# Kernel optimization log

Hardware: AMD Instinct MI355X
Metric: run time of the kernel (lower is better)

Reference implementation:

```python
import jax, jax.numpy as jnp
import numpy as np

B, L, P, A, D = 64, 512, 64, 16, 512  # batch, seq_len, n_positions, n_actions, n_lstm


def setup_inputs() -> dict:
    key = jax.random.key(0)
    ks = jax.random.split(key, 6)
    F = P + A
    observations = jax.random.normal(ks[0], (B, L, P), jnp.float32)
    actions = jax.random.normal(ks[1], (B, L, A), jnp.float32)
    # xavier_normal init as in the torch module
    W_ci = jax.random.normal(ks[2], (F, D), jnp.float32) * np.float32(np.sqrt(2.0 / (F + D)))
    b_ci = jnp.zeros((D,), jnp.float32)
    R_ig = jax.random.normal(ks[3], (D, D), jnp.float32) * np.float32(np.sqrt(2.0 / (D + D)))
    b_ig = jnp.zeros((D,), jnp.float32)
    W_out = jax.random.normal(ks[4], (D, 1), jnp.float32) * np.float32(np.sqrt(2.0 / (D + 1)))
    b_out = jnp.zeros((1,), jnp.float32)
    return dict(observations=observations, actions=actions, W_ci=W_ci, b_ci=b_ci,
                R_ig=R_ig, b_ig=b_ig, W_out=W_out, b_out=b_out)


def reference(observations, actions, W_ci, b_ci, R_ig, b_ig, W_out, b_out):
    # Custom LSTM: forget gate = 1, output gate = 1, a_out = identity =>
    #   h_t = c_t = c_{t-1} + tanh(x_t @ W_ci + b_ci) * sigmoid(h_{t-1} @ R_ig + b_ig)
    x = jnp.concatenate([observations, actions], axis=-1)          # [B, L, F]
    ci = jnp.tanh(jnp.einsum('blf,fd->bld', x, W_ci) + b_ci)       # precompute cell input [B, L, D]
    ci_seq = jnp.swapaxes(ci, 0, 1)                                # [L, B, D] for scan
    h0 = jnp.zeros((x.shape[0], R_ig.shape[0]), x.dtype)

    def step(h, ci_t):
        ig = jax.nn.sigmoid(h @ R_ig + b_ig)
        h_new = h + ci_t * ig
        return h_new, h_new

    _, hs = jax.lax.scan(step, h0, ci_seq)                         # hs: [L, B, D]
    hs = jnp.swapaxes(hs, 0, 1)                                    # [B, L, D]
    return hs @ W_out + b_out                                      # [B, L, 1]
```

## Files before the change

kernel.cpp:

```cpp
#include <hip/hip_runtime.h>


#define B_  64
#define L_  512
#define P_  64
#define A_  16
#define D_  512
#define F_  80
#define CI_R 8

#define CI_BYTES   ((size_t)B_ * L_ * D_ * 2)
#define RP_BYTES   ((size_t)D_ * D_ * 2)
#define HBUF_UINTS (2 * B_ * 2 * 256)
#define PBANK      ((size_t)B_ * 2 * 256)
#define SPIN_CAP   65536

typedef _Float16 half2_t __attribute__((ext_vector_type(2)));
typedef unsigned int uintx4 __attribute__((ext_vector_type(4)));

__device__ __forceinline__ float dot2(unsigned int r, unsigned int h, float acc) {
    return __builtin_amdgcn_fdot2(__builtin_bit_cast(half2_t, h),
                                  __builtin_bit_cast(half2_t, r), acc, false);
}
__device__ __forceinline__ float dot4u(uintx4 r, uintx4 h, float acc) {
    acc = dot2(r.x, h.x, acc);
    acc = dot2(r.y, h.y, acc);
    acc = dot2(r.z, h.z, acc);
    acc = dot2(r.w, h.w, acc);
    return acc;
}
template<int CTRL>
__device__ __forceinline__ float dpp_mov(float v) {
    return __builtin_bit_cast(float, __builtin_amdgcn_update_dpp(
        0, __builtin_bit_cast(int, v), CTRL, 0xF, 0xF, true));
}

__device__ __forceinline__ unsigned int pk_f16(float a, float b) {
    return __builtin_bit_cast(unsigned int, __builtin_amdgcn_cvt_pkrtz(a, b));
}
__device__ __forceinline__ unsigned int ld_sc01(const unsigned int* p) {
    unsigned int v;
    asm volatile("global_load_dword %0, %1, off sc0 sc1\n\t"
                 "s_waitcnt vmcnt(0)" : "=v"(v) : "v"(p) : "memory");
    return v;
}
__device__ __forceinline__ void st_sc01(unsigned int* p, unsigned int v) {
    asm volatile("global_store_dword %0, %1, off sc0 sc1" :: "v"(p), "v"(v) : "memory");
}
__device__ __forceinline__ int swz4(int i) {
    return ((i >> 3) << 3) | ((i + (i >> 3)) & 7);
}

__global__ __launch_bounds__(256) void prep_kernel(const float* __restrict__ R,
        unsigned int* __restrict__ Rp, unsigned int* __restrict__ hbuf,
        float* __restrict__ out) {
    int id = blockIdx.x * 256 + threadIdx.x;
    int dw = id & 3;
    int U = id >> 2;
    int tid_s = U & 511;
    int m  = (U >> 9) & 31;
    int qq = U >> 14;
    int w = tid_s >> 6, l = tid_s & 63, r = l >> 3, g = l & 7;
    int hh = m >> 4, j = (m >> 2) & 3, c = m & 3;
    int d  = qq * 256 + (w * 8 + r) * 4 + j;
    int k0 = hh * 256 + (g & 3) * 64 + (g >> 2) * 32 + c * 8 + 2 * dw;
    half2_t v;
    v.x = (_Float16)R[k0 * D_ + d];
    v.y = (_Float16)R[(k0 + 1) * D_ + d];
    Rp[id] = __builtin_bit_cast(unsigned int, v);
    if (id < HBUF_UINTS) hbuf[id] = 0u;
    if (id < B_ * L_) out[id] = 0.f;
}

__global__ __launch_bounds__(256) void ci_kernel(const float* __restrict__ obs,
                                                 const float* __restrict__ act,
                                                 const float* __restrict__ W,
                                                 const float* __restrict__ bci,
                                                 unsigned short* __restrict__ ci) {
    __shared__ float xs[CI_R][F_];
    int row0 = blockIdx.x * CI_R;
    int tid = threadIdx.x;
    for (int idx = tid; idx < CI_R * F_; idx += 256) {
        int r = idx / F_, f = idx % F_;
        float v = (f < P_) ? obs[(size_t)(row0 + r) * P_ + f]
                           : act[(size_t)(row0 + r) * A_ + (f - P_)];
        xs[r][f] = v;
    }
    __syncthreads();
    int d0 = tid, d1 = tid + 256;
    float a0[CI_R], a1[CI_R];
    #pragma unroll
    for (int r = 0; r < CI_R; ++r) { a0[r] = 0.f; a1[r] = 0.f; }
    for (int f = 0; f < F_; ++f) {
        float w0 = W[f * D_ + d0];
        float w1 = W[f * D_ + d1];
        #pragma unroll
        for (int r = 0; r < CI_R; ++r) {
            float xv = xs[r][f];
            a0[r] += xv * w0;
            a1[r] += xv * w1;
        }
    }
    float b0 = bci[d0], b1 = bci[d1];
    #pragma unroll
    for (int r = 0; r < CI_R; ++r) {
        float z0 = a0[r] + b0, z1 = a1[r] + b1;
        float e0 = __expf(-2.f * __builtin_fabsf(z0));
        float e1 = __expf(-2.f * __builtin_fabsf(z1));
        float m0 = (1.f - e0) * __builtin_amdgcn_rcpf(1.f + e0);
        float m1 = (1.f - e1) * __builtin_amdgcn_rcpf(1.f + e1);
        float t0 = z0 < 0.f ? -m0 : m0;
        float t1 = z1 < 0.f ? -m1 : m1;
        ci[(size_t)(row0 + r) * D_ + d0] = __builtin_bit_cast(unsigned short, (_Float16)t0);
        ci[(size_t)(row0 + r) * D_ + d1] = __builtin_bit_cast(unsigned short, (_Float16)t1);
    }
}

__global__ __launch_bounds__(512, 2)
__attribute__((amdgpu_waves_per_eu(2, 2)))
void scan_kernel(const unsigned int* __restrict__ Rp,
                 const unsigned short* __restrict__ ci,
                 const float* __restrict__ b_ig, const float* __restrict__ W_out,
                 const float* __restrict__ b_out, float* __restrict__ out,
                 unsigned int* __restrict__ hbuf)
{
    const int tid = threadIdx.x;
    const int bid = blockIdx.x;
    const int row = bid & 63;
    const int q   = bid >> 6;
    const int w = tid >> 6;
    const int l = tid & 63;
    const int r = l >> 3;
    const int g = l & 7;
    const int g3 = g & 3;

    __shared__ __align__(16) unsigned int hp2[128];
    __shared__ __align__(16) unsigned int hst[128];
    __shared__ float red[8];

    const uintx4* tb = (const uintx4*)Rp + (size_t)q * 16384 + tid;
    const int qx = q << 4;
    uintx4 rr[32];
    #pragma unroll
    for (int mm = 0; mm < 32; ++mm) rr[mm] = tb[(mm ^ qx) * 512];
    #pragma unroll
    for (int mm = 0; mm < 32; ++mm) asm volatile("" : "+v"(rr[mm]));

    const int dloc = (w * 8 + r) * 4 + g3;
    const int down = q * 256 + dloc;
    const float bg = b_ig[down];
    const float wo = W_out[down];
    const float bo = b_out[0];
    const unsigned short* cip = ci + (size_t)row * L_ * D_ + down;

    const int u_own = (w * 8 + r) * 2 + (g >> 1);
    const int wslot = swz4(u_own >> 2) * 4 + (u_own & 3);
    const int s_f = tid & 255;
    const int stslot = swz4(s_f >> 3) * 4 + ((s_f >> 1) & 3);
    const int ib = (g & 3) * 8 + (g >> 2) * 4;
    const int ri0 = swz4(ib + 0), ri1 = swz4(ib + 1);
    const int ri2 = swz4(ib + 2), ri3 = swz4(ib + 3);

    const unsigned int* rdbase = hbuf + ((size_t)row * 2 + (1 - q)) * 256 + s_f;
    unsigned int* wrbase = hbuf + ((size_t)row * 2 + q) * 256 + dloc;

    float hval = 0.f;
    __syncthreads();

    #pragma unroll 1
    for (int t = 0; t < L_; ++t) {
        unsigned short cu = cip[(size_t)t * D_];

        unsigned int vfetch = 0;
        const unsigned int* src = rdbase + (size_t)((t - 1) & 1) * PBANK;
        if (t > 0 && tid < 256) {
            asm volatile("global_load_dword %0, %1, off sc0 sc1"
                         : "=&v"(vfetch) : "v"(src) : "memory");
        }

        if (tid == 0 && t > 0) {
            float s = red[0] + red[1] + red[2] + red[3] +
                      red[4] + red[5] + red[6] + red[7];
            atomicAdd(out + row * L_ + (t - 1), s + (q == 0 ? bo : 0.f));
        }

        float p0 = 0.f, p1 = 0.f, p2 = 0.f, p3 = 0.f;

        if (t > 0) {
            const uintx4* hp4 = (const uintx4*)hp2;
            uintx4 h0 = hp4[ri0], h1 = hp4[ri1], h2 = hp4[ri2], h3 = hp4[ri3];
            p0 = dot4u(rr[0],  h0, p0); p0 = dot4u(rr[1],  h1, p0);
            p0 = dot4u(rr[2],  h2, p0); p0 = dot4u(rr[3],  h3, p0);
            p1 = dot4u(rr[4],  h0, p1); p1 = dot4u(rr[5],  h1, p1);
            p1 = dot4u(rr[6],  h2, p1); p1 = dot4u(rr[7],  h3, p1);
            p2 = dot4u(rr[8],  h0, p2); p2 = dot4u(rr[9],  h1, p2);
            p2 = dot4u(rr[10], h2, p2); p2 = dot4u(rr[11], h3, p2);
            p3 = dot4u(rr[12], h0, p3); p3 = dot4u(rr[13], h1, p3);
            p3 = dot4u(rr[14], h2, p3); p3 = dot4u(rr[15], h3, p3);
        }

        if (t > 0 && tid < 256) {
            asm volatile("s_waitcnt vmcnt(0)" : "+v"(vfetch) :: "memory");
            const unsigned int tt = (unsigned int)t;
            int it = 0;
            while ((vfetch & 0xffffu) != tt) {
                if (++it > SPIN_CAP) break;
                if (it > 2) __builtin_amdgcn_s_sleep(1);
                vfetch = ld_sc01(src);
            }
            unsigned int vo = __builtin_bit_cast(unsigned int,
                                dpp_mov<0xB1>(__builtin_bit_cast(float, vfetch)));
            if ((tid & 1) == 0)
                hst[stslot] = (vfetch >> 16) | (vo & 0xffff0000u);
        }

        asm volatile("s_waitcnt lgkmcnt(0)" ::: "memory");
        __builtin_amdgcn_s_barrier();
        asm volatile("" ::: "memory");

        if (t > 0) {
            const uintx4* hs4 = (const uintx4*)hst;
            uintx4 h0 = hs4[ri0], h1 = hs4[ri1], h2 = hs4[ri2], h3 = hs4[ri3];
            p0 = dot4u(rr[16], h0, p0); p0 = dot4u(rr[17], h1, p0);
            p0 = dot4u(rr[18], h2, p0); p0 = dot4u(rr[19], h3, p0);
            p1 = dot4u(rr[20], h0, p1); p1 = dot4u(rr[21], h1, p1);
            p1 = dot4u(rr[22], h2, p1); p1 = dot4u(rr[23], h3, p1);
            p2 = dot4u(rr[24], h0, p2); p2 = dot4u(rr[25], h1, p2);
            p2 = dot4u(rr[26], h2, p2); p2 = dot4u(rr[27], h3, p2);
            p3 = dot4u(rr[28], h0, p3); p3 = dot4u(rr[29], h1, p3);
            p3 = dot4u(rr[30], h2, p3); p3 = dot4u(rr[31], h3, p3);
        }

        float s0 = p0 + dpp_mov<0x141>(p0);
        float s1 = p1 + dpp_mov<0x141>(p1);
        float s2 = p2 + dpp_mov<0x141>(p2);
        float s3 = p3 + dpp_mov<0x141>(p3);
        s0 = s0 + dpp_mov<0xB1>(s0);  s1 = s1 + dpp_mov<0xB1>(s1);
        s2 = s2 + dpp_mov<0xB1>(s2);  s3 = s3 + dpp_mov<0xB1>(s3);
        s0 = s0 + dpp_mov<0x4E>(s0);  s1 = s1 + dpp_mov<0x4E>(s1);
        s2 = s2 + dpp_mov<0x4E>(s2);  s3 = s3 + dpp_mov<0x4E>(s3);
        float z = ((g3 & 2) ? ((g3 & 1) ? s3 : s2)
                            : ((g3 & 1) ? s1 : s0)) + bg;

        float ig  = __builtin_amdgcn_rcpf(1.f + __expf(-z));
        float civ = (float)__builtin_bit_cast(_Float16, cu);
        hval += civ * ig;

        if (g < 4) {
            unsigned int hb = pk_f16(hval, hval) & 0xffffu;
            st_sc01(wrbase + (size_t)(t & 1) * PBANK,
                    (hb << 16) | (unsigned int)(t + 1));
        }

        float po = (g < 4) ? hval * wo : 0.f;
        po += dpp_mov<0xB1>(po);
        po += dpp_mov<0x4E>(po);
        po += dpp_mov<0x141>(po);
        po += dpp_mov<0x140>(po);
        po += dpp_mov<0x142>(po);
        po += dpp_mov<0x143>(po);
        if (l == 63) red[w] = po;

        float nbh = dpp_mov<0xB1>(hval);
        if (g == 0 || g == 2) {
            hp2[wslot] = pk_f16(hval, nbh);
        }

        asm volatile("s_waitcnt lgkmcnt(0)" ::: "memory");
        __builtin_amdgcn_s_barrier();
        asm volatile("" ::: "memory");
    }

    if (tid == 0) {
        float s = red[0] + red[1] + red[2] + red[3] +
                  red[4] + red[5] + red[6] + red[7];
        atomicAdd(out + row * L_ + (L_ - 1), s + (q == 0 ? bo : 0.f));
    }
}

extern "C" void kernel_launch(void* const* d_in, const int* in_sizes, int n_in,
                              void* d_out, int out_size, void* d_ws, size_t ws_size,
                              hipStream_t stream) {
    const float* obs   = (const float*)d_in[0];
    const float* act   = (const float*)d_in[1];
    const float* W_ci  = (const float*)d_in[2];
    const float* b_ci  = (const float*)d_in[3];
    const float* R_ig  = (const float*)d_in[4];
    const float* b_ig  = (const float*)d_in[5];
    const float* W_out = (const float*)d_in[6];
    const float* b_out = (const float*)d_in[7];
    float* out = (float*)d_out;

    unsigned short* ci = (unsigned short*)d_ws;
    unsigned int* Rp   = (unsigned int*)((char*)d_ws + CI_BYTES);
    unsigned int* hbuf = (unsigned int*)((char*)d_ws + CI_BYTES + RP_BYTES);

    prep_kernel<<<512, 256, 0, stream>>>(R_ig, Rp, hbuf, out);
    ci_kernel<<<(B_ * L_) / CI_R, 256, 0, stream>>>(obs, act, W_ci, b_ci, ci);
    scan_kernel<<<B_ * 2, 512, 0, stream>>>(Rp, ci, b_ig, W_out, b_out, out, hbuf);
}
```

Measured before the change: 673.7 us.

## Batch spin-wait polls and move output reduction off the critical path

The cross-block wait loop now issues three sc0/sc1 loads back to back with short sleeps between them and checks each as it arrives. A single serialized load-and-wait per iteration is gone, which should cut the latency of detecting the partner block's h update. The per-step output projection no longer goes through a shared red[] array and a tid-0 atomic. Each wave's lane 63 now does its own atomicAdd after the barrier, so that reduction sits outside the time between the barrier and the next store. This raises the number of atomics per row-step from one per block to eight, and the spin cap semantics change.

```diff
diff --git a/kernel.cpp b/kernel.cpp
--- a/kernel.cpp
+++ b/kernel.cpp
@@ -13,7 +13,7 @@
 #define RP_BYTES   ((size_t)D_ * D_ * 2)
 #define HBUF_UINTS (2 * B_ * 2 * 256)
 #define PBANK      ((size_t)B_ * 2 * 256)
-#define SPIN_CAP   65536
+#define BATCH_CAP  4096
 
 typedef _Float16 half2_t __attribute__((ext_vector_type(2)));
 typedef unsigned int uintx4 __attribute__((ext_vector_type(4)));
@@ -37,12 +37,6 @@
 
 __device__ __forceinline__ unsigned int pk_f16(float a, float b) {
     return __builtin_bit_cast(unsigned int, __builtin_amdgcn_cvt_pkrtz(a, b));
-}
-__device__ __forceinline__ unsigned int ld_sc01(const unsigned int* p) {
-    unsigned int v;
-    asm volatile("global_load_dword %0, %1, off sc0 sc1\n\t"
-                 "s_waitcnt vmcnt(0)" : "=v"(v) : "v"(p) : "memory");
-    return v;
 }
 __device__ __forceinline__ void st_sc01(unsigned int* p, unsigned int v) {
     asm volatile("global_store_dword %0, %1, off sc0 sc1" :: "v"(p), "v"(v) : "memory");
@@ -136,7 +130,6 @@
 
     __shared__ __align__(16) unsigned int hp2[128];
     __shared__ __align__(16) unsigned int hst[128];
-    __shared__ float red[8];
 
     const uintx4* tb = (const uintx4*)Rp + (size_t)q * 16384 + tid;
     const int qx = q << 4;
@@ -176,12 +169,6 @@
         if (t > 0 && tid < 256) {
             asm volatile("global_load_dword %0, %1, off sc0 sc1"
                          : "=&v"(vfetch) : "v"(src) : "memory");
-        }
-
-        if (tid == 0 && t > 0) {
-            float s = red[0] + red[1] + red[2] + red[3] +
-                      red[4] + red[5] + red[6] + red[7];
-            atomicAdd(out + row * L_ + (t - 1), s + (q == 0 ? bo : 0.f));
         }
 
         float p0 = 0.f, p1 = 0.f, p2 = 0.f, p3 = 0.f;
@@ -202,11 +189,35 @@
         if (t > 0 && tid < 256) {
             asm volatile("s_waitcnt vmcnt(0)" : "+v"(vfetch) :: "memory");
             const unsigned int tt = (unsigned int)t;
-            int it = 0;
-            while ((vfetch & 0xffffu) != tt) {
-                if (++it > SPIN_CAP) break;
-                if (it > 2) __builtin_amdgcn_s_sleep(1);
-                vfetch = ld_sc01(src);
+            if ((vfetch & 0xffffu) != tt) {
+                int it = 0;
+                unsigned int a0, a1, a2;
+                for (;;) {
+                    asm volatile("global_load_dword %0, %1, off sc0 sc1"
+                                 : "=&v"(a0) : "v"(src) : "memory");
+                    __builtin_amdgcn_s_sleep(1);
+                    asm volatile("global_load_dword %0, %1, off sc0 sc1"
+                                 : "=&v"(a1) : "v"(src) : "memory");
+                    __builtin_amdgcn_s_sleep(1);
+                    asm volatile("global_load_dword %0, %1, off sc0 sc1"
+                                 : "=&v"(a2) : "v"(src) : "memory");
+                    asm volatile("s_waitcnt vmcnt(2)" ::: "memory");
+                    if ((a0 & 0xffffu) == tt) {
+                        vfetch = a0;
+                        asm volatile("s_waitcnt vmcnt(0)" ::: "memory");
+                        break;
+                    }
+                    asm volatile("s_waitcnt vmcnt(1)" ::: "memory");
+                    if ((a1 & 0xffffu) == tt) {
+                        vfetch = a1;
+                        asm volatile("s_waitcnt vmcnt(0)" ::: "memory");
+                        break;
+                    }
+                    asm volatile("s_waitcnt vmcnt(0)" ::: "memory");
+                    if ((a2 & 0xffffu) == tt) { vfetch = a2; break; }
+                    if (++it > BATCH_CAP) break;
+                    __builtin_amdgcn_s_sleep(1);
+                }
             }
             unsigned int vo = __builtin_bit_cast(unsigned int,
                                 dpp_mov<0xB1>(__builtin_bit_cast(float, vfetch)));
@@ -252,6 +263,15 @@
                     (hb << 16) | (unsigned int)(t + 1));
         }
 
+        float nbh = dpp_mov<0xB1>(hval);
+        if (g == 0 || g == 2) {
+            hp2[wslot] = pk_f16(hval, nbh);
+        }
+
+        asm volatile("s_waitcnt lgkmcnt(0)" ::: "memory");
+        __builtin_amdgcn_s_barrier();
+        asm volatile("" ::: "memory");
+
         float po = (g < 4) ? hval * wo : 0.f;
         po += dpp_mov<0xB1>(po);
         po += dpp_mov<0x4E>(po);
@@ -259,22 +279,10 @@
         po += dpp_mov<0x140>(po);
         po += dpp_mov<0x142>(po);
         po += dpp_mov<0x143>(po);
-        if (l == 63) red[w] = po;
-
-        float nbh = dpp_mov<0xB1>(hval);
-        if (g == 0 || g == 2) {
-            hp2[wslot] = pk_f16(hval, nbh);
-        }
-
-        asm volatile("s_waitcnt lgkmcnt(0)" ::: "memory");
-        __builtin_amdgcn_s_barrier();
-        asm volatile("" ::: "memory");
-    }
-
-    if (tid == 0) {
-        float s = red[0] + red[1] + red[2] + red[3] +
-                  red[4] + red[5] + red[6] + red[7];
-        atomicAdd(out + row * L_ + (L_ - 1), s + (q == 0 ? bo : 0.f));
+        if (l == 63) {
+            float addv = po + ((q == 0 && w == 0) ? bo : 0.f);
+            atomicAdd(out + row * L_ + t, addv);
+        }
     }
 }
 
```

After: 618.7 us. -8.2%, faster.

## Process two batch rows per scan block, halving grid and sharing registers

Applied to the files above, without the earlier changes.

Each scan workgroup now advances two batch rows together, reusing the register-resident R slice for both rows' matvecs, so the grid shrinks from 128 to 64 blocks. All 512 threads now fetch the peer half's hidden state (one row per 256-thread half). The output projection is written with per-wave atomicAdds after the barrier instead of going through a shared-memory reduction, and the spin loop sleeps after fewer polls. This doubles per-step ALU work per block but halves the number of cross-block handshakes and exposes more independent work to hide latency, at the risk of a longer critical path per step and more atomics.

```diff
diff --git a/kernel.cpp b/kernel.cpp
--- a/kernel.cpp
+++ b/kernel.cpp
@@ -49,6 +49,21 @@
 }
 __device__ __forceinline__ int swz4(int i) {
     return ((i >> 3) << 3) | ((i + (i >> 3)) & 7);
+}
+
+template<int BASE>
+__device__ __forceinline__ void dots16(const uintx4 (&rr)[32], const uintx4* h4,
+        int ri0, int ri1, int ri2, int ri3,
+        float& p0, float& p1, float& p2, float& p3) {
+    uintx4 h0 = h4[ri0], h1 = h4[ri1], h2 = h4[ri2], h3 = h4[ri3];
+    p0 = dot4u(rr[BASE + 0],  h0, p0); p0 = dot4u(rr[BASE + 1],  h1, p0);
+    p0 = dot4u(rr[BASE + 2],  h2, p0); p0 = dot4u(rr[BASE + 3],  h3, p0);
+    p1 = dot4u(rr[BASE + 4],  h0, p1); p1 = dot4u(rr[BASE + 5],  h1, p1);
+    p1 = dot4u(rr[BASE + 6],  h2, p1); p1 = dot4u(rr[BASE + 7],  h3, p1);
+    p2 = dot4u(rr[BASE + 8],  h0, p2); p2 = dot4u(rr[BASE + 9],  h1, p2);
+    p2 = dot4u(rr[BASE + 10], h2, p2); p2 = dot4u(rr[BASE + 11], h3, p2);
+    p3 = dot4u(rr[BASE + 12], h0, p3); p3 = dot4u(rr[BASE + 13], h1, p3);
+    p3 = dot4u(rr[BASE + 14], h2, p3); p3 = dot4u(rr[BASE + 15], h3, p3);
 }
 
 __global__ __launch_bounds__(256) void prep_kernel(const float* __restrict__ R,
@@ -126,17 +141,18 @@
 {
     const int tid = threadIdx.x;
     const int bid = blockIdx.x;
-    const int row = bid & 63;
-    const int q   = bid >> 6;
+    const int pr  = bid & 31;
+    const int q   = bid >> 5;
+    const int rowA = pr * 2;
+    const int rowB = pr * 2 + 1;
     const int w = tid >> 6;
     const int l = tid & 63;
     const int r = l >> 3;
     const int g = l & 7;
     const int g3 = g & 3;
 
-    __shared__ __align__(16) unsigned int hp2[128];
-    __shared__ __align__(16) unsigned int hst[128];
-    __shared__ float red[8];
+    __shared__ __align__(16) unsigned int hp2A[128], hp2B[128];
+    __shared__ __align__(16) unsigned int hstA[128], hstB[128];
 
     const uintx4* tb = (const uintx4*)Rp + (size_t)q * 16384 + tid;
     const int qx = q << 4;
@@ -151,7 +167,8 @@
     const float bg = b_ig[down];
     const float wo = W_out[down];
     const float bo = b_out[0];
-    const unsigned short* cip = ci + (size_t)row * L_ * D_ + down;
+    const unsigned short* cipA = ci + (size_t)rowA * L_ * D_ + down;
+    const unsigned short* cipB = ci + (size_t)rowB * L_ * D_ + down;
 
     const int u_own = (w * 8 + r) * 2 + (g >> 1);
     const int wslot = swz4(u_own >> 2) * 4 + (u_own & 3);
@@ -161,57 +178,48 @@
     const int ri0 = swz4(ib + 0), ri1 = swz4(ib + 1);
     const int ri2 = swz4(ib + 2), ri3 = swz4(ib + 3);
 
-    const unsigned int* rdbase = hbuf + ((size_t)row * 2 + (1 - q)) * 256 + s_f;
-    unsigned int* wrbase = hbuf + ((size_t)row * 2 + q) * 256 + dloc;
-
-    float hval = 0.f;
+    const int srow = (tid >> 8) ? rowB : rowA;
+    const unsigned int* rdbase = hbuf + ((size_t)srow * 2 + (1 - q)) * 256 + s_f;
+    unsigned int* wrA = hbuf + ((size_t)rowA * 2 + q) * 256 + dloc;
+    unsigned int* wrB = hbuf + ((size_t)rowB * 2 + q) * 256 + dloc;
+    unsigned int* hstMine = (tid >> 8) ? hstB : hstA;
+
+    float hvalA = 0.f, hvalB = 0.f;
     __syncthreads();
 
     #pragma unroll 1
     for (int t = 0; t < L_; ++t) {
-        unsigned short cu = cip[(size_t)t * D_];
+        unsigned short cuA = cipA[(size_t)t * D_];
+        unsigned short cuB = cipB[(size_t)t * D_];
 
         unsigned int vfetch = 0;
         const unsigned int* src = rdbase + (size_t)((t - 1) & 1) * PBANK;
-        if (t > 0 && tid < 256) {
+        if (t > 0) {
             asm volatile("global_load_dword %0, %1, off sc0 sc1"
                          : "=&v"(vfetch) : "v"(src) : "memory");
         }
 
-        if (tid == 0 && t > 0) {
-            float s = red[0] + red[1] + red[2] + red[3] +
-                      red[4] + red[5] + red[6] + red[7];
-            atomicAdd(out + row * L_ + (t - 1), s + (q == 0 ? bo : 0.f));
-        }
-
-        float p0 = 0.f, p1 = 0.f, p2 = 0.f, p3 = 0.f;
+        float pA0 = 0.f, pA1 = 0.f, pA2 = 0.f, pA3 = 0.f;
+        float pB0 = 0.f, pB1 = 0.f, pB2 = 0.f, pB3 = 0.f;
 
         if (t > 0) {
-            const uintx4* hp4 = (const uintx4*)hp2;
-            uintx4 h0 = hp4[ri0], h1 = hp4[ri1], h2 = hp4[ri2], h3 = hp4[ri3];
-            p0 = dot4u(rr[0],  h0, p0); p0 = dot4u(rr[1],  h1, p0);
-            p0 = dot4u(rr[2],  h2, p0); p0 = dot4u(rr[3],  h3, p0);
-            p1 = dot4u(rr[4],  h0, p1); p1 = dot4u(rr[5],  h1, p1);
-            p1 = dot4u(rr[6],  h2, p1); p1 = dot4u(rr[7],  h3, p1);
-            p2 = dot4u(rr[8],  h0, p2); p2 = dot4u(rr[9],  h1, p2);
-            p2 = dot4u(rr[10], h2, p2); p2 = dot4u(rr[11], h3, p2);
-            p3 = dot4u(rr[12], h0, p3); p3 = dot4u(rr[13], h1, p3);
-            p3 = dot4u(rr[14], h2, p3); p3 = dot4u(rr[15], h3, p3);
-        }
-
-        if (t > 0 && tid < 256) {
+            dots16<0>(rr, (const uintx4*)hp2A, ri0, ri1, ri2, ri3, pA0, pA1, pA2, pA3);
+            dots16<0>(rr, (const uintx4*)hp2B, ri0, ri1, ri2, ri3, pB0, pB1, pB2, pB3);
+        }
+
+        if (t > 0) {
             asm volatile("s_waitcnt vmcnt(0)" : "+v"(vfetch) :: "memory");
             const unsigned int tt = (unsigned int)t;
             int it = 0;
             while ((vfetch & 0xffffu) != tt) {
                 if (++it > SPIN_CAP) break;
-                if (it > 2) __builtin_amdgcn_s_sleep(1);
+                if (it > 1) __builtin_amdgcn_s_sleep(1);
                 vfetch = ld_sc01(src);
             }
             unsigned int vo = __builtin_bit_cast(unsigned int,
                                 dpp_mov<0xB1>(__builtin_bit_cast(float, vfetch)));
-            if ((tid & 1) == 0)
-                hst[stslot] = (vfetch >> 16) | (vo & 0xffff0000u);
+            if ((s_f & 1) == 0)
+                hstMine[stslot] = (vfetch >> 16) | (vo & 0xffff0000u);
         }
 
         asm volatile("s_waitcnt lgkmcnt(0)" ::: "memory");
@@ -219,62 +227,68 @@
         asm volatile("" ::: "memory");
 
         if (t > 0) {
-            const uintx4* hs4 = (const uintx4*)hst;
-            uintx4 h0 = hs4[ri0], h1 = hs4[ri1], h2 = hs4[ri2], h3 = hs4[ri3];
-            p0 = dot4u(rr[16], h0, p0); p0 = dot4u(rr[17], h1, p0);
-            p0 = dot4u(rr[18], h2, p0); p0 = dot4u(rr[19], h3, p0);
-            p1 = dot4u(rr[20], h0, p1); p1 = dot4u(rr[21], h1, p1);
-            p1 = dot4u(rr[22], h2, p1); p1 = dot4u(rr[23], h3, p1);
-            p2 = dot4u(rr[24], h0, p2); p2 = dot4u(rr[25], h1, p2);
-            p2 = dot4u(rr[26], h2, p2); p2 = dot4u(rr[27], h3, p2);
-            p3 = dot4u(rr[28], h0, p3); p3 = dot4u(rr[29], h1, p3);
-            p3 = dot4u(rr[30], h2, p3); p3 = dot4u(rr[31], h3, p3);
-        }
-
-        float s0 = p0 + dpp_mov<0x141>(p0);
-        float s1 = p1 + dpp_mov<0x141>(p1);
-        float s2 = p2 + dpp_mov<0x141>(p2);
-        float s3 = p3 + dpp_mov<0x141>(p3);
-        s0 = s0 + dpp_mov<0xB1>(s0);  s1 = s1 + dpp_mov<0xB1>(s1);
-        s2 = s2 + dpp_mov<0xB1>(s2);  s3 = s3 + dpp_mov<0xB1>(s3);
-        s0 = s0 + dpp_mov<0x4E>(s0);  s1 = s1 + dpp_mov<0x4E>(s1);
-        s2 = s2 + dpp_mov<0x4E>(s2);  s3 = s3 + dpp_mov<0x4E>(s3);
-        float z = ((g3 & 2) ? ((g3 & 1) ? s3 : s2)
-                            : ((g3 & 1) ? s1 : s0)) + bg;
-
-        float ig  = __builtin_amdgcn_rcpf(1.f + __expf(-z));
-        float civ = (float)__builtin_bit_cast(_Float16, cu);
-        hval += civ * ig;
+            dots16<16>(rr, (const uintx4*)hstA, ri0, ri1, ri2, ri3, pA0, pA1, pA2, pA3);
+            dots16<16>(rr, (const uintx4*)hstB, ri0, ri1, ri2, ri3, pB0, pB1, pB2, pB3);
+        }
+
+        float sA0 = pA0 + dpp_mov<0x141>(pA0);
+        float sA1 = pA1 + dpp_mov<0x141>(pA1);
+        float sA2 = pA2 + dpp_mov<0x141>(pA2);
+        float sA3 = pA3 + dpp_mov<0x141>(pA3);
+        float sB0 = pB0 + dpp_mov<0x141>(pB0);
+        float sB1 = pB1 + dpp_mov<0x141>(pB1);
+        float sB2 = pB2 + dpp_mov<0x141>(pB2);
+        float sB3 = pB3 + dpp_mov<0x141>(pB3);
+        sA0 = sA0 + dpp_mov<0xB1>(sA0);  sA1 = sA1 + dpp_mov<0xB1>(sA1);
+        sA2 = sA2 + dpp_mov<0xB1>(sA2);  sA3 = sA3 + dpp_mov<0xB1>(sA3);
+        sB0 = sB0 + dpp_mov<0xB1>(sB0);  sB1 = sB1 + dpp_mov<0xB1>(sB1);
+        sB2 = sB2 + dpp_mov<0xB1>(sB2);  sB3 = sB3 + dpp_mov<0xB1>(sB3);
+        sA0 = sA0 + dpp_mov<0x4E>(sA0);  sA1 = sA1 + dpp_mov<0x4E>(sA1);
+        sA2 = sA2 + dpp_mov<0x4E>(sA2);  sA3 = sA3 + dpp_mov<0x4E>(sA3);
+        sB0 = sB0 + dpp_mov<0x4E>(sB0);  sB1 = sB1 + dpp_mov<0x4E>(sB1);
+        sB2 = sB2 + dpp_mov<0x4E>(sB2);  sB3 = sB3 + dpp_mov<0x4E>(sB3);
+        float zA = ((g3 & 2) ? ((g3 & 1) ? sA3 : sA2)
+                             : ((g3 & 1) ? sA1 : sA0)) + bg;
+        float zB = ((g3 & 2) ? ((g3 & 1) ? sB3 : sB2)
+                             : ((g3 & 1) ? sB1 : sB0)) + bg;
+
+        float igA  = __builtin_amdgcn_rcpf(1.f + __expf(-zA));
+        float igB  = __builtin_amdgcn_rcpf(1.f + __expf(-zB));
+        hvalA += (float)__builtin_bit_cast(_Float16, cuA) * igA;
+        hvalB += (float)__builtin_bit_cast(_Float16, cuB) * igB;
 
         if (g < 4) {
-            unsigned int hb = pk_f16(hval, hval) & 0xffffu;
-            st_sc01(wrbase + (size_t)(t & 1) * PBANK,
-                    (hb << 16) | (unsigned int)(t + 1));
-        }
-
-        float po = (g < 4) ? hval * wo : 0.f;
-        po += dpp_mov<0xB1>(po);
-        po += dpp_mov<0x4E>(po);
-        po += dpp_mov<0x141>(po);
-        po += dpp_mov<0x140>(po);
-        po += dpp_mov<0x142>(po);
-        po += dpp_mov<0x143>(po);
-        if (l == 63) red[w] = po;
-
-        float nbh = dpp_mov<0xB1>(hval);
+            unsigned int tag = (unsigned int)(t + 1);
+            st_sc01(wrA + (size_t)(t & 1) * PBANK,
+                    ((pk_f16(hvalA, hvalA) & 0xffffu) << 16) | tag);
+            st_sc01(wrB + (size_t)(t & 1) * PBANK,
+                    ((pk_f16(hvalB, hvalB) & 0xffffu) << 16) | tag);
+        }
+
+        float nbhA = dpp_mov<0xB1>(hvalA);
+        float nbhB = dpp_mov<0xB1>(hvalB);
         if (g == 0 || g == 2) {
-            hp2[wslot] = pk_f16(hval, nbh);
+            hp2A[wslot] = pk_f16(hvalA, nbhA);
+            hp2B[wslot] = pk_f16(hvalB, nbhB);
         }
 
         asm volatile("s_waitcnt lgkmcnt(0)" ::: "memory");
         __builtin_amdgcn_s_barrier();
         asm volatile("" ::: "memory");
-    }
-
-    if (tid == 0) {
-        float s = red[0] + red[1] + red[2] + red[3] +
-                  red[4] + red[5] + red[6] + red[7];
-        atomicAdd(out + row * L_ + (L_ - 1), s + (q == 0 ? bo : 0.f));
+
+        float poA = (g < 4) ? hvalA * wo : 0.f;
+        float poB = (g < 4) ? hvalB * wo : 0.f;
+        poA += dpp_mov<0xB1>(poA);   poB += dpp_mov<0xB1>(poB);
+        poA += dpp_mov<0x4E>(poA);   poB += dpp_mov<0x4E>(poB);
+        poA += dpp_mov<0x141>(poA);  poB += dpp_mov<0x141>(poB);
+        poA += dpp_mov<0x140>(poA);  poB += dpp_mov<0x140>(poB);
+        poA += dpp_mov<0x142>(poA);  poB += dpp_mov<0x142>(poB);
+        poA += dpp_mov<0x143>(poA);  poB += dpp_mov<0x143>(poB);
+        if (l == 63) {
+            float ex = (q == 0 && w == 0) ? bo : 0.f;
+            atomicAdd(out + rowA * L_ + t, poA + ex);
+            atomicAdd(out + rowB * L_ + t, poB + ex);
+        }
     }
 }
 
@@ -297,5 +311,5 @@
 
     prep_kernel<<<512, 256, 0, stream>>>(R_ig, Rp, hbuf, out);
     ci_kernel<<<(B_ * L_) / CI_R, 256, 0, stream>>>(obs, act, W_ci, b_ci, ci);
-    scan_kernel<<<B_ * 2, 512, 0, stream>>>(Rp, ci, b_ig, W_out, b_out, out, hbuf);
-}
+    scan_kernel<<<B_, 512, 0, stream>>>(Rp, ci, b_ig, W_out, b_out, out, hbuf);
+}
```

Result: slower. 1.147 ms (+70.3%).
